# Optimization experiments

Measured on AMD Instinct MI355X. Metric: run time of the kernel, lower is better.

Reference implementation:

```python
import jax, jax.numpy as jnp
import numpy as np

DIM = 256
HEADS = 8
HEAD_DIM = DIM // HEADS
B = 4
Wd, Hd = 48, 48
N = Wd * Hd  # 2304


def _layernorm(x, g, b, eps=1e-5):
    mu = jnp.mean(x, axis=-1, keepdims=True)
    var = jnp.mean(jnp.square(x - mu), axis=-1, keepdims=True)
    return (x - mu) * jax.lax.rsqrt(var + eps) * g + b


def _build_mask(mask):
    # Binarize: <1 -> 0, >0 -> 1 (identity on {0,1} inputs)
    m = (mask > 0).astype(jnp.float32)
    flat = m.reshape(B, m.shape[1], Hd * Wd)[:, 0, :]  # [B, N]
    # mask[b,i,j] zeroed where (flat[j]==0 & flat[i]==1) | (flat[j]==0 & flat[i]==0)
    col0 = flat[:, None, :] == 0   # varies along j
    row = flat[:, :, None]         # varies along i
    bad = (col0 & (row == 1)) | (col0 & (row == 0))
    return (~bad).astype(jnp.float32)  # [B, N, N]


def setup_inputs() -> dict:
    key = jax.random.key(0)
    ks = jax.random.split(key, 12)
    s = 0.02
    x = jax.random.normal(ks[0], (B, N, DIM), jnp.float32)
    mask = jax.random.randint(ks[1], (B, 1, Wd, Hd), 0, 2).astype(jnp.float32)
    inp = {
        "x": x,
        "mask": mask,
        "ln_g": jnp.ones((DIM,), jnp.float32),
        "ln_b": jnp.zeros((DIM,), jnp.float32),
        "Wq": jax.random.normal(ks[2], (DIM, DIM), jnp.float32) * s,
        "bq": jnp.zeros((DIM,), jnp.float32),
        "Wk": jax.random.normal(ks[3], (DIM, DIM), jnp.float32) * s,
        "bk": jnp.zeros((DIM,), jnp.float32),
        "Wv": jax.random.normal(ks[4], (DIM, DIM), jnp.float32) * s,
        "bv": jnp.zeros((DIM,), jnp.float32),
        "Wp": jax.random.normal(ks[5], (DIM, DIM), jnp.float32) * s,
        "bp": jnp.zeros((DIM,), jnp.float32),
    }
    return inp


def reference(x, mask, ln_g, ln_b, Wq, bq, Wk, bk, Wv, bv, Wp, bp):
    Bx, Nx, C = x.shape
    mask_f = _build_mask(mask)  # [B, N, N]
    xn = _layernorm(x, ln_g, ln_b)
    def heads(Wm, bm):
        return (xn @ Wm + bm).reshape(Bx, Nx, HEADS, HEAD_DIM).transpose(0, 2, 1, 3)
    q = heads(Wq, bq)
    k = heads(Wk, bk)
    v = heads(Wv, bv)
    # NOTE: no 1/sqrt(d) scaling in the original; multiplicative 0/1 mask pre-softmax
    attn = jnp.einsum("bhnd,bhmd->bhnm", q, k) * mask_f[:, None, :, :]
    attn = jax.nn.softmax(attn, axis=-1)
    out = jnp.einsum("bhnm,bhmd->bhnd", attn, v)
    out = out.transpose(0, 2, 1, 3).reshape(Bx, Nx, C)
    return out @ Wp + bp
```

## Files before the change

kernel.cpp:

```cpp
#include <hip/hip_runtime.h>
#include <math.h>

typedef __attribute__((ext_vector_type(8))) short short8;
typedef __attribute__((ext_vector_type(4))) float f32x4;

#if __has_builtin(__builtin_amdgcn_exp2f)
#define EXP2F(x) __builtin_amdgcn_exp2f(x)
#else
#define EXP2F(x) exp2f(x)
#endif

constexpr int B   = 4;
constexpr int N   = 2304;
constexpr int DIM = 256;
constexpr int NH  = 8;
constexpr int DH  = 32;
constexpr int M   = B * N;
constexpr int SLOTS = 2336;
constexpr int CST = SLOTS * DH;
constexpr int XPB = SLOTS * DIM;
constexpr float LOG2E = 1.44269504088896f;

__device__ inline unsigned short f2bf(float f) {
    union { float f; unsigned u; } c; c.f = f;
    unsigned u = c.u;
    u += 0x7fffu + ((u >> 16) & 1u);
    return (unsigned short)(u >> 16);
}
__device__ inline float bf2f(unsigned short h) {
    union { unsigned u; float f; } c; c.u = ((unsigned)h) << 16;
    return c.f;
}
__device__ inline unsigned bits(float f) {
    union { float f; unsigned u; } c; c.f = f; return c.u;
}

__device__ inline size_t fo256(int r, int k) {
    return ((size_t)((r >> 4) * 8 + (k >> 5)) << 9)
         + (size_t)(((((k & 31) >> 3) << 4) + (r & 15)) * 8 + (k & 7));
}
__device__ inline size_t foQK(int n, int d) {
    return ((size_t)(n >> 4) << 9)
         + (size_t)((((d >> 3) << 4) + (n & 15)) * 8 + (d & 7));
}
__device__ inline size_t foKI(int slot, int d) {
    int tile = ((slot >> 5) << 1) + (slot & 1);
    int npos = (slot & 31) >> 1;
    return ((size_t)tile << 9)
         + (size_t)((((d >> 3) << 4) + npos) * 8 + (d & 7));
}
__device__ inline size_t foVTC(int d, int key) {
    return ((size_t)((d >> 4) * (SLOTS / 32) + (key >> 5)) << 9)
         + (size_t)(((((key & 31) >> 3) << 4) + (d & 15)) * 8 + (key & 7));
}

__global__ __launch_bounds__(256) void prep_kernel(
    const float* __restrict__ x, const float* __restrict__ g,
    const float* __restrict__ bta, unsigned short* __restrict__ xh,
    const float* __restrict__ Wq, const float* __restrict__ Wk,
    const float* __restrict__ Wv, const float* __restrict__ Wp,
    unsigned short* __restrict__ Wth, unsigned short* __restrict__ Wtl,
    const float* __restrict__ mask, int* __restrict__ inv,
    int* __restrict__ ncp, float* __restrict__ vm)
{
    __shared__ float tbuf[32][33];
    __shared__ int wsum[4];
    int bx = blockIdx.x;
    int t = threadIdx.x;
    if (bx < 2304) {
        int wave = t >> 6, lane = t & 63;
        int row = bx * 4 + wave;
        float4 v = *(const float4*)&x[(size_t)row * DIM + lane * 4];
        float s = v.x + v.y + v.z + v.w;
        #pragma unroll
        for (int o = 32; o > 0; o >>= 1) s += __shfl_xor(s, o, 64);
        float mu = s * (1.0f / DIM);
        float d0 = v.x - mu, d1 = v.y - mu, d2 = v.z - mu, d3 = v.w - mu;
        float s2 = d0 * d0 + d1 * d1 + d2 * d2 + d3 * d3;
        #pragma unroll
        for (int o = 32; o > 0; o >>= 1) s2 += __shfl_xor(s2, o, 64);
        float r = rsqrtf(s2 * (1.0f / DIM) + 1e-5f);
        float4 gg = *(const float4*)&g[lane * 4];
        float4 bb = *(const float4*)&bta[lane * 4];
        ushort4 hi;
        hi.x = f2bf(d0 * r * gg.x + bb.x);
        hi.y = f2bf(d1 * r * gg.y + bb.y);
        hi.z = f2bf(d2 * r * gg.z + bb.z);
        hi.w = f2bf(d3 * r * gg.w + bb.w);
        *(ushort4*)&xh[fo256(row, lane * 4)] = hi;
    } else if (bx < 2560) {
        int idx = bx - 2304;
        int z = idx >> 6, w = idx & 63;
        const float* W = (z == 0) ? Wq : (z == 1) ? Wk : (z == 2) ? Wv : Wp;
        unsigned short* oh = Wth + (size_t)z * DIM * DIM;
        unsigned short* ol = Wtl + (size_t)z * DIM * DIM;
        int tx = t & 31, ty0 = t >> 5;
        int n0 = (w & 7) * 32, k0 = (w >> 3) * 32;
        for (int ty = ty0; ty < 32; ty += 8)
            tbuf[ty][tx] = W[(size_t)(k0 + ty) * DIM + n0 + tx];
        __syncthreads();
        for (int nn = ty0; nn < 32; nn += 8) {
            float v = tbuf[tx][nn];
            unsigned short hh = f2bf(v);
            size_t o = fo256(n0 + nn, k0 + tx);
            oh[o] = hh;
            ol[o] = f2bf(v - bf2f(hh));
        }
    } else {
        int b = bx - 2560;
        int wave = t >> 6, lane = t & 63;
        vm[b * 256 + t] = 0.f;
        int cnt = 0;
        for (int j = t; j < N; j += 256) cnt += (mask[(size_t)b * N + j] > 0.f);
        #pragma unroll
        for (int o = 32; o > 0; o >>= 1) cnt += __shfl_down(cnt, o, 64);
        if (lane == 0) wsum[wave] = cnt;
        __syncthreads();
        int Nc = wsum[0] + wsum[1] + wsum[2] + wsum[3];
        int Nkp = (Nc + 31) & ~31;
        if (t == 0) { ncp[b * 2] = Nc; ncp[b * 2 + 1] = Nkp; }
        int baseK = 0;
        for (int j0 = 0; j0 < N; j0 += 256) {
            int j = j0 + t;
            bool keep = mask[(size_t)b * N + j] > 0.f;
            unsigned long long bal = __ballot(keep);
            int pos = __popcll(bal & ((1ull << lane) - 1ull));
            int wc  = __popcll(bal);
            __syncthreads();
            if (lane == 0) wsum[wave] = wc;
            __syncthreads();
            int wb = 0;
            for (int w = 0; w < wave; ++w) wb += wsum[w];
            int tot = wsum[0] + wsum[1] + wsum[2] + wsum[3];
            int keptBefore = baseK + wb + pos;
            if (keep) inv[(size_t)b * SLOTS + keptBefore] = j;
            else      inv[(size_t)b * SLOTS + Nkp + (j - keptBefore)] = j;
            baseK += tot;
        }
    }
}

__global__ __launch_bounds__(256) void permute_x(
    const unsigned short* __restrict__ xh,
    const int* __restrict__ inv, const int* __restrict__ ncp,
    unsigned short* __restrict__ xph)
{
    int tid = threadIdx.x;
    int wave = tid >> 6, lane = tid & 63;
    int kq = lane >> 4, r = lane & 15;
    int rtg = blockIdx.x * 4 + wave;
    int b = rtg / (SLOTS / 16), rt = rtg % (SLOTS / 16);
    int y = blockIdx.y;
    unsigned short* dst = xph + (size_t)b * XPB;
    int slot = rt * 16 + r;
    int Nc = ncp[b * 2], Nkp = ncp[b * 2 + 1];
    int mend = Nkp + (N - Nc);
    bool pad = (slot >= Nc && slot < Nkp) || slot >= mend;
    int n = pad ? -1 : inv[(size_t)b * SLOTS + slot];
    #pragma unroll
    for (int kt = 0; kt < 4; ++kt) {
        int k0 = (y * 4 + kt) * 32;
        short8 v = {0, 0, 0, 0, 0, 0, 0, 0};
        if (n >= 0) {
            int gn = b * N + n;
            v = *(const short8*)&xh[(((size_t)(gn >> 4) * 8 + (k0 >> 5)) << 9)
                                    + (kq * 16 + (gn & 15)) * 8];
        }
        *(short8*)&dst[(((size_t)(rt * 8 + (k0 >> 5))) << 9) + lane * 8] = v;
    }
}

__global__ __launch_bounds__(256, 8) void gemm_qkv(
    const unsigned short* __restrict__ xh,
    const unsigned short* __restrict__ xph,
    const unsigned short* __restrict__ Wth,
    const float* __restrict__ bq, const float* __restrict__ bk,
    const float* __restrict__ bv, const int* __restrict__ ncp,
    unsigned short* __restrict__ qb, unsigned short* __restrict__ kc,
    unsigned short* __restrict__ vc, float* __restrict__ vm)
{
    constexpr size_t WSZ = (size_t)DIM * DIM;
    int z = blockIdx.z, bx = blockIdx.x;
    int tid = threadIdx.x;
    int wave = tid >> 6, lane = tid & 63;
    int quad = lane >> 4, l16 = lane & 15;
    const unsigned short *PA, *PB;
    int arow0, brow0, b;
    if (z == 0) {
        if (bx >= 576) return;
        arow0 = (bx >> 3) * 128 + wave * 32;
        brow0 = (bx & 7) * 32;
        b = ((bx >> 3) * 128) / N;
        PA = xh; PB = Wth;
    } else if (z == 1) {
        b = bx / 152;
        int rr = bx % 152;
        arow0 = (rr >> 3) * 128 + wave * 32;
        brow0 = (rr & 7) * 32;
        if (arow0 >= SLOTS) return;
        if (arow0 >= ncp[b * 2 + 1]) return;
        PA = xph + (size_t)b * XPB;
        PB = Wth + WSZ;
    } else {
        if (bx >= 584) return;
        int nidx = bx % 292;
        b = nidx / 73;
        arow0 = (bx / 292) * 128 + wave * 32;
        brow0 = (nidx % 73) * 32;
        PA = Wth + 2 * WSZ;
        PB = xph + (size_t)b * XPB;
    }
    f32x4 acc[2][2] = {};
    #pragma unroll
    for (int k0 = 0; k0 < DIM; k0 += 32) {
        size_t at = (((size_t)(arow0 >> 4) * 8 + (k0 >> 5)) << 9) + lane * 8;
        size_t bt = (((size_t)(brow0 >> 4) * 8 + (k0 >> 5)) << 9) + lane * 8;
        short8 a0 = *(const short8*)&PA[at];
        short8 a1 = *(const short8*)&PA[at + 4096];
        short8 b0 = *(const short8*)&PB[bt];
        short8 b1 = *(const short8*)&PB[bt + 4096];
        acc[0][0] = __builtin_amdgcn_mfma_f32_16x16x32_bf16(a0, b0, acc[0][0], 0, 0, 0);
        acc[0][1] = __builtin_amdgcn_mfma_f32_16x16x32_bf16(a0, b1, acc[0][1], 0, 0, 0);
        acc[1][0] = __builtin_amdgcn_mfma_f32_16x16x32_bf16(a1, b0, acc[1][0], 0, 0, 0);
        acc[1][1] = __builtin_amdgcn_mfma_f32_16x16x32_bf16(a1, b1, acc[1][1], 0, 0, 0);
    }
    if (z == 0) {
        int nbase = arow0 - b * N;
        #pragma unroll
        for (int j = 0; j < 2; ++j) {
            int c = brow0 + j * 16 + l16;
            int h = c >> 5, d = c & 31;
            float bs = bq[c];
            unsigned short* ob = qb + (size_t)(b * NH + h) * ((size_t)N * DH);
            #pragma unroll
            for (int i = 0; i < 2; ++i)
            #pragma unroll
            for (int r = 0; r < 4; ++r) {
                int n = nbase + i * 16 + quad * 4 + r;
                ob[foQK(n, d)] = f2bf((acc[i][j][r] + bs) * LOG2E);
            }
        }
    } else if (z == 1) {
        #pragma unroll
        for (int j = 0; j < 2; ++j) {
            int c = brow0 + j * 16 + l16;
            int h = c >> 5, d = c & 31;
            float bs = bk[c];
            unsigned short* ob = kc + (size_t)(b * NH + h) * CST;
            #pragma unroll
            for (int i = 0; i < 2; ++i)
            #pragma unroll
            for (int r = 0; r < 4; ++r) {
                int slot = arow0 + i * 16 + quad * 4 + r;
                ob[foKI(slot, d)] = f2bf(acc[i][j][r] + bs);
            }
        }
    } else {
        int Nc  = ncp[b * 2];
        int Nkp = ncp[b * 2 + 1];
        int mend = Nkp + (N - Nc);
        bool anymask = (brow0 + 32 > Nkp) && (brow0 < mend);
        #pragma unroll
        for (int i = 0; i < 2; ++i)
        #pragma unroll
        for (int r = 0; r < 4; ++r) {
            int m = arow0 + i * 16 + quad * 4 + r;
            int h = m >> 5, d = m & 31;
            float bs = bv[m];
            unsigned short* ob = vc + (size_t)(b * NH + h) * CST;
            float vsum = 0.f;
            #pragma unroll
            for (int j = 0; j < 2; ++j) {
                int key = brow0 + j * 16 + l16;
                float val = acc[i][j][r] + bs;
                if (key < Nkp) ob[foVTC(d, key)] = f2bf(val);
                else if (key < mend) vsum += val;
            }
            if (anymask) {
                vsum += __shfl_xor(vsum, 1, 64);
                vsum += __shfl_xor(vsum, 2, 64);
                vsum += __shfl_xor(vsum, 4, 64);
                vsum += __shfl_xor(vsum, 8, 64);
                if (l16 == 0) atomicAdd(&vm[(size_t)(b * NH + h) * 32 + d], vsum);
            }
        }
    }
}

__global__ __launch_bounds__(128, 4) void attn_kernel(
    const unsigned short* __restrict__ Qb,
    const unsigned short* __restrict__ Kc,
    const unsigned short* __restrict__ Vc,
    const int* __restrict__ ncp,
    const float* __restrict__ vm,
    unsigned short* __restrict__ ah)
{
    __shared__ unsigned short pbuf[2 * 2 * 640];
    int tid  = threadIdx.x;
    int wave = tid >> 6, lane = tid & 63;
    int quad = lane >> 4, l16 = lane & 15;
    int bh = blockIdx.y, b = bh >> 3, h = bh & 7;

    int q0 = (blockIdx.x * 2 + wave) * 32;
    const unsigned short* Qf = Qb + (size_t)bh * ((size_t)N * DH);
    const unsigned short* Kf = Kc + (size_t)bh * CST;
    const unsigned short* Vf = Vc + (size_t)bh * CST;

    int Nc  = ncp[b * 2];
    int Nkp = ncp[b * 2 + 1];
    int kend = Nkp;

    short8 qA0 = *(const short8*)&Qf[((size_t)(q0 >> 4) << 9) + lane * 8];
    short8 qA1 = *(const short8*)&Qf[((size_t)((q0 >> 4) + 1) << 9) + lane * 8];

    f32x4 o00 = {0,0,0,0}, o01 = {0,0,0,0}, o10 = {0,0,0,0}, o11 = {0,0,0,0};
    float l0[4] = {0,0,0,0}, l1[4] = {0,0,0,0};

    unsigned short* pb0 = &pbuf[(wave * 2 + 0) * 640];
    unsigned short* pb1 = &pbuf[(wave * 2 + 1) * 640];

    short8 kB0 = *(const short8*)&Kf[lane * 8];
    short8 kB1 = *(const short8*)&Kf[512 + lane * 8];
    short8 vB0 = *(const short8*)&Vf[lane * 8];
    short8 vB1 = *(const short8*)&Vf[((size_t)(SLOTS / 32) << 9) + lane * 8];

    for (int k0 = 0; k0 < kend; k0 += 32) {
        int kn = (k0 + 32 < kend) ? k0 + 32 : 0;
        short8 nk0 = *(const short8*)&Kf[((size_t)(kn >> 4) << 9) + lane * 8];
        short8 nk1 = *(const short8*)&Kf[((size_t)((kn >> 4) + 1) << 9) + lane * 8];
        short8 nv0 = *(const short8*)&Vf[((size_t)(kn >> 5) << 9) + lane * 8];
        short8 nv1 = *(const short8*)&Vf[((size_t)((SLOTS / 32) + (kn >> 5)) << 9) + lane * 8];

        int key0 = k0 + 2 * l16;
        bool in0 = key0 < Nc;
        bool in1 = key0 + 1 < Nc;
        f32x4 z = {0,0,0,0};
        f32x4 s00 = __builtin_amdgcn_mfma_f32_16x16x32_bf16(qA0, kB0, z, 0, 0, 0);
        f32x4 s01 = __builtin_amdgcn_mfma_f32_16x16x32_bf16(qA0, kB1, z, 0, 0, 0);
        f32x4 s10 = __builtin_amdgcn_mfma_f32_16x16x32_bf16(qA1, kB0, z, 0, 0, 0);
        f32x4 s11 = __builtin_amdgcn_mfma_f32_16x16x32_bf16(qA1, kB1, z, 0, 0, 0);
        #pragma unroll
        for (int r = 0; r < 4; ++r) {
            int row = quad * 4 + r;
            float p00 = in0 ? EXP2F(s00[r]) : 0.f;
            float p01 = in1 ? EXP2F(s01[r]) : 0.f;
            float p10 = in0 ? EXP2F(s10[r]) : 0.f;
            float p11 = in1 ? EXP2F(s11[r]) : 0.f;
            l0[r] += p00 + p01;
            l1[r] += p10 + p11;
            unsigned pk0 = (bits(p00) >> 16) | (bits(p01) & 0xffff0000u);
            unsigned pk1 = (bits(p10) >> 16) | (bits(p11) & 0xffff0000u);
            *(unsigned*)&pb0[row * 40 + 2 * l16] = pk0;
            *(unsigned*)&pb1[row * 40 + 2 * l16] = pk1;
        }
        short8 pA0 = *(const short8*)&pb0[l16 * 40 + quad * 8];
        short8 pA1 = *(const short8*)&pb1[l16 * 40 + quad * 8];
        o00 = __builtin_amdgcn_mfma_f32_16x16x32_bf16(pA0, vB0, o00, 0, 0, 0);
        o01 = __builtin_amdgcn_mfma_f32_16x16x32_bf16(pA0, vB1, o01, 0, 0, 0);
        o10 = __builtin_amdgcn_mfma_f32_16x16x32_bf16(pA1, vB0, o10, 0, 0, 0);
        o11 = __builtin_amdgcn_mfma_f32_16x16x32_bf16(pA1, vB1, o11, 0, 0, 0);

        kB0 = nk0; kB1 = nk1; vB0 = nv0; vB1 = nv1;
    }
    #pragma unroll
    for (int r = 0; r < 4; ++r) {
        #pragma unroll
        for (int off = 1; off < 16; off <<= 1) {
            l0[r] += __shfl_xor(l0[r], off, 64);
            l1[r] += __shfl_xor(l1[r], off, 64);
        }
    }
    float vm0 = vm[bh * 32 + l16];
    float vm1 = vm[bh * 32 + 16 + l16];
    float lext = (float)(N - Nc);
    #pragma unroll
    for (int r = 0; r < 4; ++r) {
        int row = quad * 4 + r;
        float ia = 1.f / (l0[r] + lext);
        float ib = 1.f / (l1[r] + lext);
        int ra = b * N + q0 + row;
        int rb = ra + 16;
        ah[fo256(ra, h * 32 + l16)]      = f2bf((o00[r] + vm0) * ia);
        ah[fo256(ra, h * 32 + 16 + l16)] = f2bf((o01[r] + vm1) * ia);
        ah[fo256(rb, h * 32 + l16)]      = f2bf((o10[r] + vm0) * ib);
        ah[fo256(rb, h * 32 + 16 + l16)] = f2bf((o11[r] + vm1) * ib);
    }
}

__global__ __launch_bounds__(256, 8) void gemm_p(
    const unsigned short* __restrict__ Ahi,
    const unsigned short* __restrict__ Wth, const unsigned short* __restrict__ Wtl,
    const float* __restrict__ bias, float* __restrict__ out)
{
    constexpr size_t WSZ = (size_t)DIM * DIM;
    const unsigned short* Bhi = Wth + 3 * WSZ;
    const unsigned short* Blo = Wtl + 3 * WSZ;
    int tid = threadIdx.x;
    int wave = tid >> 6, lane = tid & 63;
    int quad = lane >> 4, l16 = lane & 15;
    int r0 = blockIdx.y * 128 + wave * 32;
    int c0 = blockIdx.x * 16;
    f32x4 acc0 = {}, acc1 = {};
    #pragma unroll
    for (int k0 = 0; k0 < DIM; k0 += 32) {
        size_t at = (((size_t)(r0 >> 4) * 8 + (k0 >> 5)) << 9) + lane * 8;
        size_t bt = (((size_t)(c0 >> 4) * 8 + (k0 >> 5)) << 9) + lane * 8;
        short8 ah0 = *(const short8*)&Ahi[at];
        short8 ah1 = *(const short8*)&Ahi[at + 4096];
        short8 bh = *(const short8*)&Bhi[bt];
        short8 bl = *(const short8*)&Blo[bt];
        acc0 = __builtin_amdgcn_mfma_f32_16x16x32_bf16(ah0, bh, acc0, 0, 0, 0);
        acc0 = __builtin_amdgcn_mfma_f32_16x16x32_bf16(ah0, bl, acc0, 0, 0, 0);
        acc1 = __builtin_amdgcn_mfma_f32_16x16x32_bf16(ah1, bh, acc1, 0, 0, 0);
        acc1 = __builtin_amdgcn_mfma_f32_16x16x32_bf16(ah1, bl, acc1, 0, 0, 0);
    }
    int c = c0 + l16;
    float bs = bias[c];
    #pragma unroll
    for (int r = 0; r < 4; ++r) {
        int R0 = r0 + quad * 4 + r;
        out[(size_t)R0 * DIM + c] = acc0[r] + bs;
        out[(size_t)(R0 + 16) * DIM + c] = acc1[r] + bs;
    }
}

extern "C" void kernel_launch(void* const* d_in, const int* in_sizes, int n_in,
                              void* d_out, int out_size, void* d_ws, size_t ws_size,
                              hipStream_t stream)
{
    const float* x    = (const float*)d_in[0];
    const float* mask = (const float*)d_in[1];
    const float* ln_g = (const float*)d_in[2];
    const float* ln_b = (const float*)d_in[3];
    const float* Wq   = (const float*)d_in[4];
    const float* bq   = (const float*)d_in[5];
    const float* Wk   = (const float*)d_in[6];
    const float* bk   = (const float*)d_in[7];
    const float* Wv   = (const float*)d_in[8];
    const float* bv   = (const float*)d_in[9];
    const float* Wp   = (const float*)d_in[10];
    const float* bp   = (const float*)d_in[11];
    float* out = (float*)d_out;

    constexpr size_t SZ  = (size_t)M * DIM;
    constexpr size_t CSZ = (size_t)B * NH * CST;
    constexpr size_t XSZ = (size_t)B * XPB;
    constexpr size_t WSZ = (size_t)DIM * DIM;
    unsigned short* p = (unsigned short*)d_ws;
    unsigned short* xh = p;  p += SZ;
    unsigned short* xph = p; p += XSZ;
    unsigned short* qb = p;  p += SZ;
    unsigned short* kc = p;  p += CSZ;
    unsigned short* vc = p;  p += CSZ;
    unsigned short* ah = p;  p += SZ;
    unsigned short* wth = p; p += 4 * WSZ;
    unsigned short* wtl = p; p += 4 * WSZ;
    float* vm = (float*)p;
    int* inv = (int*)(vm + (size_t)B * NH * 32);
    int* ncp = inv + (size_t)B * SLOTS;

    prep_kernel<<<2564, 256, 0, stream>>>(
        x, ln_g, ln_b, xh, Wq, Wk, Wv, Wp, wth, wtl, mask, inv, ncp, vm);

    permute_x<<<dim3((B * (SLOTS / 16)) / 4, 2), 256, 0, stream>>>(
        xh, inv, ncp, xph);

    gemm_qkv<<<dim3(608, 1, 3), 256, 0, stream>>>(
        xh, xph, wth, bq, bk, bv, ncp, qb, kc, vc, vm);

    attn_kernel<<<dim3(N / 64, B * NH), 128, 0, stream>>>(
        qb, kc, vc, ncp, vm, ah);

    gemm_p<<<dim3(DIM / 16, M / 128), 256, 0, stream>>>(
        ah, wth, wtl, bp, out);
}
```

Measured before the change: 152.3 us.

## Scatter LN output directly into permuted layout and split attention keys across waves

The mask compaction now computes a forward slot map in a small setup kernel and zero-fills the padding slots. The layernorm kernel then writes each normalized row both to the normal layout and to its permuted slot, which removes the separate permute_x gather pass. The attention kernel also changes from two waves handling different query tiles to two waves splitting the key range for the same 32 queries. Their partial outputs and row sums are combined through shared memory, which doubles the grid to raise parallelism at the cost of an LDS reduction and a barrier.

```diff
diff --git a/kernel.cpp b/kernel.cpp
--- a/kernel.cpp
+++ b/kernel.cpp
@@ -54,43 +54,20 @@
          + (size_t)(((((key & 31) >> 3) << 4) + (d & 15)) * 8 + (key & 7));
 }
 
-__global__ __launch_bounds__(256) void prep_kernel(
-    const float* __restrict__ x, const float* __restrict__ g,
-    const float* __restrict__ bta, unsigned short* __restrict__ xh,
+__global__ __launch_bounds__(256) void setup_kernel(
     const float* __restrict__ Wq, const float* __restrict__ Wk,
     const float* __restrict__ Wv, const float* __restrict__ Wp,
     unsigned short* __restrict__ Wth, unsigned short* __restrict__ Wtl,
-    const float* __restrict__ mask, int* __restrict__ inv,
-    int* __restrict__ ncp, float* __restrict__ vm)
+    const float* __restrict__ mask, int* __restrict__ ncp,
+    int* __restrict__ fwd, float* __restrict__ vm,
+    unsigned short* __restrict__ xph)
 {
     __shared__ float tbuf[32][33];
     __shared__ int wsum[4];
     int bx = blockIdx.x;
     int t = threadIdx.x;
-    if (bx < 2304) {
-        int wave = t >> 6, lane = t & 63;
-        int row = bx * 4 + wave;
-        float4 v = *(const float4*)&x[(size_t)row * DIM + lane * 4];
-        float s = v.x + v.y + v.z + v.w;
-        #pragma unroll
-        for (int o = 32; o > 0; o >>= 1) s += __shfl_xor(s, o, 64);
-        float mu = s * (1.0f / DIM);
-        float d0 = v.x - mu, d1 = v.y - mu, d2 = v.z - mu, d3 = v.w - mu;
-        float s2 = d0 * d0 + d1 * d1 + d2 * d2 + d3 * d3;
-        #pragma unroll
-        for (int o = 32; o > 0; o >>= 1) s2 += __shfl_xor(s2, o, 64);
-        float r = rsqrtf(s2 * (1.0f / DIM) + 1e-5f);
-        float4 gg = *(const float4*)&g[lane * 4];
-        float4 bb = *(const float4*)&bta[lane * 4];
-        ushort4 hi;
-        hi.x = f2bf(d0 * r * gg.x + bb.x);
-        hi.y = f2bf(d1 * r * gg.y + bb.y);
-        hi.z = f2bf(d2 * r * gg.z + bb.z);
-        hi.w = f2bf(d3 * r * gg.w + bb.w);
-        *(ushort4*)&xh[fo256(row, lane * 4)] = hi;
-    } else if (bx < 2560) {
-        int idx = bx - 2304;
-        int z = idx >> 6, w = idx & 63;
+    if (bx < 256) {
+        int z = bx >> 6, w = bx & 63;
         const float* W = (z == 0) ? Wq : (z == 1) ? Wk : (z == 2) ? Wv : Wp;
         unsigned short* oh = Wth + (size_t)z * DIM * DIM;
         unsigned short* ol = Wtl + (size_t)z * DIM * DIM;
@@ -107,7 +84,7 @@
             ol[o] = f2bf(v - bf2f(hh));
         }
     } else {
-        int b = bx - 2560;
+        int b = bx - 256;
         int wave = t >> 6, lane = t & 63;
         vm[b * 256 + t] = 0.f;
         int cnt = 0;
@@ -118,6 +95,7 @@
         __syncthreads();
         int Nc = wsum[0] + wsum[1] + wsum[2] + wsum[3];
         int Nkp = (Nc + 31) & ~31;
+        int mend = Nkp + (N - Nc);
         if (t == 0) { ncp[b * 2] = Nc; ncp[b * 2 + 1] = Nkp; }
         int baseK = 0;
         for (int j0 = 0; j0 < N; j0 += 256) {
@@ -133,41 +111,51 @@
             for (int w = 0; w < wave; ++w) wb += wsum[w];
             int tot = wsum[0] + wsum[1] + wsum[2] + wsum[3];
             int keptBefore = baseK + wb + pos;
-            if (keep) inv[(size_t)b * SLOTS + keptBefore] = j;
-            else      inv[(size_t)b * SLOTS + Nkp + (j - keptBefore)] = j;
+            fwd[(size_t)b * N + j] = keep ? keptBefore
+                                          : Nkp + (j - keptBefore);
             baseK += tot;
         }
-    }
-}
-
-__global__ __launch_bounds__(256) void permute_x(
-    const unsigned short* __restrict__ xh,
-    const int* __restrict__ inv, const int* __restrict__ ncp,
-    unsigned short* __restrict__ xph)
-{
-    int tid = threadIdx.x;
-    int wave = tid >> 6, lane = tid & 63;
-    int kq = lane >> 4, r = lane & 15;
-    int rtg = blockIdx.x * 4 + wave;
-    int b = rtg / (SLOTS / 16), rt = rtg % (SLOTS / 16);
-    int y = blockIdx.y;
-    unsigned short* dst = xph + (size_t)b * XPB;
-    int slot = rt * 16 + r;
-    int Nc = ncp[b * 2], Nkp = ncp[b * 2 + 1];
-    int mend = Nkp + (N - Nc);
-    bool pad = (slot >= Nc && slot < Nkp) || slot >= mend;
-    int n = pad ? -1 : inv[(size_t)b * SLOTS + slot];
-    #pragma unroll
-    for (int kt = 0; kt < 4; ++kt) {
-        int k0 = (y * 4 + kt) * 32;
-        short8 v = {0, 0, 0, 0, 0, 0, 0, 0};
-        if (n >= 0) {
-            int gn = b * N + n;
-            v = *(const short8*)&xh[(((size_t)(gn >> 4) * 8 + (k0 >> 5)) << 9)
-                                    + (kq * 16 + (gn & 15)) * 8];
-        }
-        *(short8*)&dst[(((size_t)(rt * 8 + (k0 >> 5))) << 9) + lane * 8] = v;
-    }
+        int c1 = Nkp - Nc;
+        unsigned short* xb = xph + (size_t)b * XPB;
+        for (int u = t; u < 32 * 64; u += 256) {
+            int pi = u >> 6;
+            int kk = (u & 63) * 4;
+            int slot = (pi < c1) ? (Nc + pi) : (mend + (pi - c1));
+            ushort4 z4 = {0, 0, 0, 0};
+            *(ushort4*)&xb[fo256(slot, kk)] = z4;
+        }
+    }
+}
+
+__global__ __launch_bounds__(256) void ln_kernel(
+    const float* __restrict__ x, const float* __restrict__ g,
+    const float* __restrict__ bta, const int* __restrict__ fwd,
+    unsigned short* __restrict__ xh, unsigned short* __restrict__ xph)
+{
+    int t = threadIdx.x;
+    int wave = t >> 6, lane = t & 63;
+    int row = blockIdx.x * 4 + wave;
+    float4 v = *(const float4*)&x[(size_t)row * DIM + lane * 4];
+    float s = v.x + v.y + v.z + v.w;
+    #pragma unroll
+    for (int o = 32; o > 0; o >>= 1) s += __shfl_xor(s, o, 64);
+    float mu = s * (1.0f / DIM);
+    float d0 = v.x - mu, d1 = v.y - mu, d2 = v.z - mu, d3 = v.w - mu;
+    float s2 = d0 * d0 + d1 * d1 + d2 * d2 + d3 * d3;
+    #pragma unroll
+    for (int o = 32; o > 0; o >>= 1) s2 += __shfl_xor(s2, o, 64);
+    float r = rsqrtf(s2 * (1.0f / DIM) + 1e-5f);
+    float4 gg = *(const float4*)&g[lane * 4];
+    float4 bb = *(const float4*)&bta[lane * 4];
+    ushort4 hi;
+    hi.x = f2bf(d0 * r * gg.x + bb.x);
+    hi.y = f2bf(d1 * r * gg.y + bb.y);
+    hi.z = f2bf(d2 * r * gg.z + bb.z);
+    hi.w = f2bf(d3 * r * gg.w + bb.w);
+    *(ushort4*)&xh[fo256(row, lane * 4)] = hi;
+    int b = row / N;
+    int slot = fwd[row];
+    *(ushort4*)&xph[(size_t)b * XPB + fo256(slot, lane * 4)] = hi;
 }
 
 __global__ __launch_bounds__(256, 8) void gemm_qkv(
@@ -296,19 +284,22 @@
     unsigned short* __restrict__ ah)
 {
     __shared__ unsigned short pbuf[2 * 2 * 640];
+    __shared__ float cbuf[64 * 24];
     int tid  = threadIdx.x;
-    int wave = tid >> 6, lane = tid & 63;
+    int kh   = tid >> 6, lane = tid & 63;
     int quad = lane >> 4, l16 = lane & 15;
     int bh = blockIdx.y, b = bh >> 3, h = bh & 7;
 
-    int q0 = (blockIdx.x * 2 + wave) * 32;
+    int q0 = blockIdx.x * 32;
     const unsigned short* Qf = Qb + (size_t)bh * ((size_t)N * DH);
     const unsigned short* Kf = Kc + (size_t)bh * CST;
     const unsigned short* Vf = Vc + (size_t)bh * CST;
 
     int Nc  = ncp[b * 2];
     int Nkp = ncp[b * 2 + 1];
-    int kend = Nkp;
+    int chunks = Nkp >> 5;
+    int kbeg = ((chunks * kh) >> 1) << 5;
+    int kend = ((chunks * (kh + 1)) >> 1) << 5;
 
     short8 qA0 = *(const short8*)&Qf[((size_t)(q0 >> 4) << 9) + lane * 8];
     short8 qA1 = *(const short8*)&Qf[((size_t)((q0 >> 4) + 1) << 9) + lane * 8];
@@ -316,16 +307,16 @@
     f32x4 o00 = {0,0,0,0}, o01 = {0,0,0,0}, o10 = {0,0,0,0}, o11 = {0,0,0,0};
     float l0[4] = {0,0,0,0}, l1[4] = {0,0,0,0};
 
-    unsigned short* pb0 = &pbuf[(wave * 2 + 0) * 640];
-    unsigned short* pb1 = &pbuf[(wave * 2 + 1) * 640];
-
-    short8 kB0 = *(const short8*)&Kf[lane * 8];
-    short8 kB1 = *(const short8*)&Kf[512 + lane * 8];
-    short8 vB0 = *(const short8*)&Vf[lane * 8];
-    short8 vB1 = *(const short8*)&Vf[((size_t)(SLOTS / 32) << 9) + lane * 8];
-
-    for (int k0 = 0; k0 < kend; k0 += 32) {
-        int kn = (k0 + 32 < kend) ? k0 + 32 : 0;
+    unsigned short* pb0 = &pbuf[(kh * 2 + 0) * 640];
+    unsigned short* pb1 = &pbuf[(kh * 2 + 1) * 640];
+
+    short8 kB0 = *(const short8*)&Kf[((size_t)(kbeg >> 4) << 9) + lane * 8];
+    short8 kB1 = *(const short8*)&Kf[((size_t)((kbeg >> 4) + 1) << 9) + lane * 8];
+    short8 vB0 = *(const short8*)&Vf[((size_t)(kbeg >> 5) << 9) + lane * 8];
+    short8 vB1 = *(const short8*)&Vf[((size_t)((SLOTS / 32) + (kbeg >> 5)) << 9) + lane * 8];
+
+    for (int k0 = kbeg; k0 < kend; k0 += 32) {
+        int kn = (k0 + 32 < kend) ? k0 + 32 : kbeg;
         short8 nk0 = *(const short8*)&Kf[((size_t)(kn >> 4) << 9) + lane * 8];
         short8 nk1 = *(const short8*)&Kf[((size_t)((kn >> 4) + 1) << 9) + lane * 8];
         short8 nv0 = *(const short8*)&Vf[((size_t)(kn >> 5) << 9) + lane * 8];
@@ -369,6 +360,26 @@
             l0[r] += __shfl_xor(l0[r], off, 64);
             l1[r] += __shfl_xor(l1[r], off, 64);
         }
+    }
+    if (kh == 1) {
+        float* cb = &cbuf[lane * 24];
+        *(f32x4*)&cb[0]  = o00;
+        *(f32x4*)&cb[4]  = o01;
+        *(f32x4*)&cb[8]  = o10;
+        *(f32x4*)&cb[12] = o11;
+        #pragma unroll
+        for (int r = 0; r < 4; ++r) { cb[16 + r] = l0[r]; cb[20 + r] = l1[r]; }
+    }
+    __syncthreads();
+    if (kh == 1) return;
+    {
+        float* cb = &cbuf[lane * 24];
+        o00 += *(f32x4*)&cb[0];
+        o01 += *(f32x4*)&cb[4];
+        o10 += *(f32x4*)&cb[8];
+        o11 += *(f32x4*)&cb[12];
+        #pragma unroll
+        for (int r = 0; r < 4; ++r) { l0[r] += cb[16 + r]; l1[r] += cb[20 + r]; }
     }
     float vm0 = vm[bh * 32 + l16];
     float vm1 = vm[bh * 32 + 16 + l16];
@@ -456,19 +467,19 @@
     unsigned short* wth = p; p += 4 * WSZ;
     unsigned short* wtl = p; p += 4 * WSZ;
     float* vm = (float*)p;
-    int* inv = (int*)(vm + (size_t)B * NH * 32);
-    int* ncp = inv + (size_t)B * SLOTS;
-
-    prep_kernel<<<2564, 256, 0, stream>>>(
-        x, ln_g, ln_b, xh, Wq, Wk, Wv, Wp, wth, wtl, mask, inv, ncp, vm);
-
-    permute_x<<<dim3((B * (SLOTS / 16)) / 4, 2), 256, 0, stream>>>(
-        xh, inv, ncp, xph);
+    int* ncp = (int*)(vm + (size_t)B * NH * 32);
+    int* fwd = ncp + 2 * B;
+
+    setup_kernel<<<260, 256, 0, stream>>>(
+        Wq, Wk, Wv, Wp, wth, wtl, mask, ncp, fwd, vm, xph);
+
+    ln_kernel<<<2304, 256, 0, stream>>>(
+        x, ln_g, ln_b, fwd, xh, xph);
 
     gemm_qkv<<<dim3(608, 1, 3), 256, 0, stream>>>(
         xh, xph, wth, bq, bk, bv, ncp, qb, kc, vc, vm);
 
-    attn_kernel<<<dim3(N / 64, B * NH), 128, 0, stream>>>(
+    attn_kernel<<<dim3(N / 32, B * NH), 128, 0, stream>>>(
         qb, kc, vc, ncp, vm, ah);
 
     gemm_p<<<dim3(DIM / 16, M / 128), 256, 0, stream>>>(
```

Measured after the change: 150.7 us. No clear change (-1.0%).
